# Kernel tuning notes

Hardware: AMD Instinct MI355X
Metric: run time of the kernel (lower is better)

Reference implementation:

```python
import jax, jax.numpy as jnp
import numpy as np
import math

NUM_HEADS = 3
WINDOW = 7


def _shift_masks(ws):
    # row_mask: block mask for windows wrapping across the bottom edge
    half = ws * (ws // 2)  # 21 for ws=7
    row = np.zeros((ws * ws, ws * ws), np.float32)
    row[-half:, :-half] = -np.inf
    row[:-half, -half:] = -np.inf
    # column_mask = rearrange(row, '(r w1) (c w2) -> (w1 r) (w2 c)')
    col = row.reshape(ws, ws, ws, ws).transpose(1, 0, 3, 2).reshape(ws * ws, ws * ws)
    return jnp.asarray(row), jnp.asarray(col)


def setup_inputs() -> dict:
    key = jax.random.key(0)
    ks = jax.random.split(key, 5)
    B, S, E = 64, 3136, 96
    return {
        'x': jax.random.normal(ks[0], (B, S, E), jnp.float32),
        'w1': jax.random.normal(ks[1], (3 * E, E), jnp.float32) * 0.05,
        'b1': jax.random.normal(ks[2], (3 * E,), jnp.float32) * 0.05,
        'w2': jax.random.normal(ks[3], (E, E), jnp.float32) * 0.05,
        'b2': jax.random.normal(ks[4], (E,), jnp.float32) * 0.05,
    }


def reference(x, w1, b1, w2, b2):
    b, S, E = x.shape
    h = w = int(math.sqrt(S))          # 56
    ws = WINDOW
    H = NUM_HEADS
    Eh = E // H                        # head dim = 32
    nh, nw = h // ws, w // ws          # windows per axis = 8
    scale = 1.0 / math.sqrt(E / H)
    # faithful to original: forward shift = -ws//2 = -4, inverse shift = ws//2 = 3
    shift_fwd = -ws // 2
    shift_bwd = ws // 2

    qkv = x @ w1.T + b1                              # [b, S, 3E]
    qkv = qkv.reshape(b, h, w, E, 3)                 # (c K) split, K fastest
    qkv = jnp.roll(qkv, (shift_fwd, shift_fwd), axis=(1, 2))
    # b (nh m1) (nw m2) (H Eh) K -> b H nh nw (m1 m2) Eh K
    qkv = qkv.reshape(b, nh, ws, nw, ws, H, Eh, 3)
    qkv = qkv.transpose(0, 5, 1, 3, 2, 4, 6, 7).reshape(b, H, nh, nw, ws * ws, Eh, 3)
    Q, K, V = qkv[..., 0], qkv[..., 1], qkv[..., 2]

    s = jnp.einsum('bHhwme,bHhwne->bHhwmn', Q, K) * scale  # [b,H,nh,nw,49,49]
    row_mask, col_mask = _shift_masks(ws)
    s = s.at[:, :, -1, :].add(row_mask)   # last row of windows
    s = s.at[:, :, :, -1].add(col_mask)   # last column of windows

    att = jax.nn.softmax(s, axis=-1)
    o = jnp.einsum('bHhwmn,bHhwne->bHhwme', att, V)        # [b,H,nh,nw,49,Eh]
    # b H nh nw (m1 m2) Eh -> b (nh m1) (nw m2) (H Eh)
    o = o.reshape(b, H, nh, nw, ws, ws, Eh)
    o = o.transpose(0, 2, 4, 3, 5, 1, 6).reshape(b, h, w, E)
    o = jnp.roll(o, (shift_bwd, shift_bwd), axis=(1, 2))
    o = o.reshape(b, S, E)
    return o @ w2.T + b2
```

## Files before the change

### kernel.cpp

```cpp
#include <hip/hip_runtime.h>


typedef _Float16 f16;
typedef _Float16 f16x2 __attribute__((ext_vector_type(2)));
typedef _Float16 f16x4 __attribute__((ext_vector_type(4)));
typedef _Float16 f16x8 __attribute__((ext_vector_type(8)));
typedef float f32x4 __attribute__((ext_vector_type(4)));

static __device__ __forceinline__ f32x4 mfma16(f16x8 a, f16x8 b, f32x4 c) {
    return __builtin_amdgcn_mfma_f32_16x16x32_f16(a, b, c, 0, 0, 0);
}
static __device__ __forceinline__ f16x8 cvt8(const float* __restrict__ p) {
    float4 f0 = *(const float4*)(p);
    float4 f1 = *(const float4*)(p + 4);
    f16x8 h;
    h[0]=(f16)f0.x; h[1]=(f16)f0.y; h[2]=(f16)f0.z; h[3]=(f16)f0.w;
    h[4]=(f16)f1.x; h[5]=(f16)f1.y; h[6]=(f16)f1.z; h[7]=(f16)f1.w;
    return h;
}
static __device__ __forceinline__ f16x8 cvt8p(const float4& f0, const float4& f1) {
    f16x8 h;
    h[0]=(f16)f0.x; h[1]=(f16)f0.y; h[2]=(f16)f0.z; h[3]=(f16)f0.w;
    h[4]=(f16)f1.x; h[5]=(f16)f1.y; h[6]=(f16)f1.z; h[7]=(f16)f1.w;
    return h;
}

#define SMEM_BYTES 31152
#define OFF_K  10192
#define OFF_VT 20384

union U2 { int i; f16x2 h; };
union U8 { int i[4]; f16x8 h; };

template<bool WS>
__global__ __launch_bounds__(256, 4) void swin_fused(
    const float* __restrict__ x, const float* __restrict__ w1,
    const float* __restrict__ b1, const float* __restrict__ w2,
    const float* __restrict__ b2, float* __restrict__ out,
    const f16* __restrict__ w1p, const f16* __restrict__ w2p,
    const float* __restrict__ b1p)
{
    __shared__ __align__(16) char smem[SMEM_BYTES];
    f16* q_s  = (f16*)(smem);
    f16* k_s  = (f16*)(smem + OFF_K);
    f16* vt_s = (f16*)(smem + OFF_VT);
    f16* o_s  = q_s;

    const int tid  = threadIdx.x;
    const int wv   = tid >> 6;
    const int lane = tid & 63;
    const int lrow = lane & 15;
    const int lq   = lane >> 4;

    const int bx = blockIdx.x;
    const int b  = bx >> 6;
    const int wz = bx & 63;
    const int wh = wz >> 3;
    const int ww = wz & 7;

    const float* xb = x + b * (3136 * 96);

    if (tid < 96) {
        #pragma unroll
        for (int p7 = 49; p7 < 56; ++p7) vt_s[tid * 56 + p7] = (f16)0.f;
    }
    if (tid < 8) vt_s[96 * 56 + tid] = (f16)0.f;

    {
        f16x8 bf[5][3];
        int   kq[5], cb[5];
        #pragma unroll
        for (int t = 0; t < 5; ++t) {
            int ot = wv + 4 * t;
            if (ot < 18) {
                int kqv = ot / 6;
                kq[t] = kqv;
                cb[t] = (ot - kqv * 6) * 16;
                if constexpr (WS) {
                    #pragma unroll
                    for (int ks = 0; ks < 3; ++ks)
                        bf[t][ks] = *(const f16x8*)(w1p + (ot*16 + lrow)*96 + ks*32 + lq*8);
                } else {
                    int srowA = (ot*16 + lrow - kqv*96) * 3 + kqv;
                    #pragma unroll
                    for (int ks = 0; ks < 3; ++ks)
                        bf[t][ks] = cvt8(w1 + srowA*96 + ks*32 + lq*8);
                }
            } else kq[t] = -1;
        }
        const float* xrow[4];
        #pragma unroll
        for (int pt = 0; pt < 4; ++pt) {
            int p  = pt * 16 + lrow;
            int pc = (p < 49) ? p : 48;
            int i  = pc / 7, j = pc - i * 7;
            int r  = wh * 7 + i + 4; if (r >= 56) r -= 56;
            int c  = ww * 7 + j + 4; if (c >= 56) c -= 56;
            xrow[pt] = xb + (r * 56 + c) * 96;
        }
        float4 xbuf0[3][2], xbuf1[3][2];
        #pragma unroll
        for (int ks = 0; ks < 3; ++ks) {
            xbuf0[ks][0] = *(const float4*)(xrow[0] + ks * 32 + lq * 8);
            xbuf0[ks][1] = *(const float4*)(xrow[0] + ks * 32 + lq * 8 + 4);
        }
        #pragma unroll
        for (int pt = 0; pt < 4; ++pt) {
            float4 (*cur)[2] = (pt & 1) ? xbuf1 : xbuf0;
            float4 (*nxt)[2] = (pt & 1) ? xbuf0 : xbuf1;
            if (pt < 3) {
                #pragma unroll
                for (int ks = 0; ks < 3; ++ks) {
                    nxt[ks][0] = *(const float4*)(xrow[pt+1] + ks * 32 + lq * 8);
                    nxt[ks][1] = *(const float4*)(xrow[pt+1] + ks * 32 + lq * 8 + 4);
                }
            }
            f16x8 xf[3];
            #pragma unroll
            for (int ks = 0; ks < 3; ++ks) xf[ks] = cvt8p(cur[ks][0], cur[ks][1]);
            const int  p   = pt * 16 + lrow;
            const bool pok = (p < 49);
            #pragma unroll
            for (int t = 0; t < 5; ++t) {
                if (kq[t] < 0) continue;
                int ot = wv + 4 * t;
                f32x4 acc = {0.f, 0.f, 0.f, 0.f};
                if (kq[t] == 2) {
                    #pragma unroll
                    for (int ks = 0; ks < 3; ++ks) acc = mfma16(xf[ks], bf[t][ks], acc);
                    float bc;
                    if constexpr (WS) bc = b1p[ot*16 + lrow];
                    else              bc = b1[(ot*16 + lrow - 192)*3 + 2];
                    int cc = cb[t] + lrow;
                    f16x4 pk;
                    #pragma unroll
                    for (int i2 = 0; i2 < 4; ++i2) pk[i2] = (f16)(acc[i2] + bc);
                    int p4 = pt * 16 + lq * 4;
                    if (p4 < 45)       *(f16x4*)(vt_s + cc * 56 + p4) = pk;
                    else if (p4 == 48) vt_s[cc * 56 + 48] = pk[0];
                } else {
                    #pragma unroll
                    for (int ks = 0; ks < 3; ++ks) acc = mfma16(bf[t][ks], xf[ks], acc);
                    if (pok) {
                        f32x4 br;
                        if constexpr (WS) {
                            br = *(const f32x4*)(b1p + ot*16 + lq*4);
                        } else {
                            #pragma unroll
                            for (int i2 = 0; i2 < 4; ++i2)
                                br[i2] = b1[(ot*16 + lq*4 + i2 - kq[t]*96)*3 + kq[t]];
                        }
                        f16x4 pk;
                        #pragma unroll
                        for (int i2 = 0; i2 < 4; ++i2) pk[i2] = (f16)(acc[i2] + br[i2]);
                        f16* dst = (kq[t] == 0 ? q_s : k_s) + p * 104 + cb[t] + lq * 4;
                        *(f16x4*)dst = pk;
                    }
                }
            }
        }
    }
    __syncthreads();

    const bool mrow = (wh == 7), mcol = (ww == 7);
    const float scale = 0.17677669529663687f;
    const int m = wv * 16 + lrow;

    float mv[16];
    {
        const bool am = (m >= 28);
        const bool a4 = (m % 7) >= 4;
        #pragma unroll
        for (int nt = 0; nt < 4; ++nt)
            #pragma unroll
            for (int i2 = 0; i2 < 4; ++i2) {
                int nn = nt * 16 + lq * 4 + i2;
                bool ok = (nn < 49)
                       && (!mrow || (am == (nn >= 28)))
                       && (!mcol || (a4 == ((nn % 7) >= 4)));
                mv[nt*4 + i2] = ok ? 0.f : -3e38f;
            }
    }
    const int idxA = lrow + 32 * (lq & 1);
    const int idxB = idxA + 16;

    f16x8 bq[3];
    #pragma unroll
    for (int hh = 0; hh < 3; ++hh)
        bq[hh] = *(const f16x8*)(q_s + m * 104 + hh * 32 + lq * 8);

    f32x4 sc[4];
    #pragma unroll
    for (int nt = 0; nt < 4; ++nt) {
        f16x8 ak = *(const f16x8*)(k_s + (nt*16 + lrow)*104 + lq*8);
        f32x4 z = {0.f, 0.f, 0.f, 0.f};
        sc[nt] = mfma16(ak, bq[0], z);
    }

    #pragma unroll
    for (int hh = 0; hh < 3; ++hh) {
        f16x8 akn[4];
        if (hh < 2) {
            #pragma unroll
            for (int nt = 0; nt < 4; ++nt)
                akn[nt] = *(const f16x8*)(k_s + (nt*16 + lrow)*104 + (hh+1)*32 + lq*8);
        }
        f16x8 va[2][2];
        #pragma unroll
        for (int et = 0; et < 2; ++et) {
            int vrow = hh * 32 + et * 16 + lrow;
            va[et][0] = *(const f16x8*)(vt_s + vrow * 56 + lq * 8);
            va[et][1] = *(const f16x8*)(vt_s + vrow * 56 + 32 + lq * 8);
        }
        float ev[16];
        #pragma unroll
        for (int nt = 0; nt < 4; ++nt)
            #pragma unroll
            for (int i2 = 0; i2 < 4; ++i2)
                ev[nt*4 + i2] = fmaf(sc[nt][i2], scale, mv[nt*4 + i2]);
        float tm[8];
        #pragma unroll
        for (int k2 = 0; k2 < 8; ++k2) tm[k2] = fmaxf(ev[2*k2], ev[2*k2+1]);
        #pragma unroll
        for (int k2 = 0; k2 < 4; ++k2) tm[k2] = fmaxf(tm[k2], tm[k2+4]);
        float vm = fmaxf(fmaxf(tm[0], tm[1]), fmaxf(tm[2], tm[3]));
        vm = fmaxf(vm, __shfl_xor(vm, 16));
        vm = fmaxf(vm, __shfl_xor(vm, 32));
        #pragma unroll
        for (int k2 = 0; k2 < 16; ++k2) ev[k2] = __expf(ev[k2] - vm);
        float ts[8];
        #pragma unroll
        for (int k2 = 0; k2 < 8; ++k2) ts[k2] = ev[2*k2] + ev[2*k2+1];
        #pragma unroll
        for (int k2 = 0; k2 < 4; ++k2) ts[k2] += ts[k2+4];
        float s = (ts[0] + ts[1]) + (ts[2] + ts[3]);
        s += __shfl_xor(s, 16);
        s += __shfl_xor(s, 32);
        float inv = 1.0f / s;

        int pd[4][2];
        #pragma unroll
        for (int nt = 0; nt < 4; ++nt) {
            U2 u0, u1;
            u0.h[0] = (f16)ev[nt*4+0]; u0.h[1] = (f16)ev[nt*4+1];
            u1.h[0] = (f16)ev[nt*4+2]; u1.h[1] = (f16)ev[nt*4+3];
            pd[nt][0] = u0.i; pd[nt][1] = u1.i;
        }
        U8 ub0, ub1;
        #pragma unroll
        for (int w = 0; w < 4; ++w) {
            int idx = (w < 2) ? idxA : idxB;
            int rr  = w & 1;
            int a0v = __shfl(pd[0][rr], idx);
            int a1v = __shfl(pd[1][rr], idx);
            ub0.i[w] = (lq & 2) ? a1v : a0v;
            int c0v = __shfl(pd[2][rr], idx);
            int c1v = __shfl(pd[3][rr], idx);
            ub1.i[w] = (lq & 2) ? c1v : c0v;
        }
        #pragma unroll
        for (int et = 0; et < 2; ++et) {
            f32x4 z = {0.f, 0.f, 0.f, 0.f};
            f32x4 oc = mfma16(va[et][0], ub0.h, z);
            oc = mfma16(va[et][1], ub1.h, oc);
            if (m < 49) {
                f16x4 pk;
                #pragma unroll
                for (int i2 = 0; i2 < 4; ++i2) pk[i2] = (f16)(oc[i2] * inv);
                *(f16x4*)(o_s + m * 104 + hh * 32 + et * 16 + lq * 4) = pk;
            }
        }
        if (hh < 2) {
            #pragma unroll
            for (int nt = 0; nt < 4; ++nt) {
                f32x4 z = {0.f, 0.f, 0.f, 0.f};
                sc[nt] = mfma16(akn[nt], bq[hh+1], z);
            }
        }
    }

    {
        f16x8 bo[3];
        #pragma unroll
        for (int ks = 0; ks < 3; ++ks)
            bo[ks] = *(const f16x8*)(o_s + m * 104 + ks * 32 + lq * 8);
        int mm2 = (m < 49) ? m : 48;
        int i = mm2 / 7, j = mm2 - i * 7;
        int orow = wh * 7 + i + 3; if (orow >= 56) orow -= 56;
        int ocol = ww * 7 + j + 3; if (ocol >= 56) ocol -= 56;
        float* op = out + (size_t)(b * 3136 + orow * 56 + ocol) * 96;

        f16x8 aw0[3], aw1[3];
        #pragma unroll
        for (int ks = 0; ks < 3; ++ks) {
            if constexpr (WS)
                aw0[ks] = *(const f16x8*)(w2p + lrow*96 + ks*32 + lq*8);
            else
                aw0[ks] = cvt8(w2 + lrow*96 + ks*32 + lq*8);
        }
        #pragma unroll
        for (int ot2 = 0; ot2 < 6; ++ot2) {
            f16x8* cw = (ot2 & 1) ? aw1 : aw0;
            f16x8* nw = (ot2 & 1) ? aw0 : aw1;
            if (ot2 < 5) {
                #pragma unroll
                for (int ks = 0; ks < 3; ++ks) {
                    if constexpr (WS)
                        nw[ks] = *(const f16x8*)(w2p + ((ot2+1)*16 + lrow)*96 + ks*32 + lq*8);
                    else
                        nw[ks] = cvt8(w2 + ((ot2+1)*16 + lrow)*96 + ks*32 + lq*8);
                }
            }
            f32x4 acc = {0.f, 0.f, 0.f, 0.f};
            #pragma unroll
            for (int ks = 0; ks < 3; ++ks) acc = mfma16(cw[ks], bo[ks], acc);
            f32x4 bias = *(const f32x4*)(b2 + ot2 * 16 + lq * 4);
            if (m < 49) {
                f32x4 o4 = acc + bias;
                *(f32x4*)(op + ot2 * 16 + lq * 4) = o4;
            }
        }
    }
}

__global__ void prep_weights(const float* __restrict__ w1, const float* __restrict__ b1,
                             const float* __restrict__ w2,
                             f16* __restrict__ w1p, f16* __restrict__ w2p,
                             float* __restrict__ b1p)
{
    int idx = blockIdx.x * 256 + threadIdx.x;
    if (idx < 27648) {
        int np = idx / 96, k = idx - np * 96;
        int kq = np / 96, c96 = np - kq * 96;
        w1p[idx] = (f16)w1[(c96 * 3 + kq) * 96 + k];
    } else if (idx < 36864) {
        int i2 = idx - 27648;
        w2p[i2] = (f16)w2[i2];
    } else if (idx < 37152) {
        int np = idx - 36864;
        int kq = np / 96, c96 = np - kq * 96;
        b1p[np] = b1[c96 * 3 + kq];
    }
}

extern "C" void kernel_launch(void* const* d_in, const int* in_sizes, int n_in,
                              void* d_out, int out_size, void* d_ws, size_t ws_size,
                              hipStream_t stream) {
    const float* x  = (const float*)d_in[0];
    const float* w1 = (const float*)d_in[1];
    const float* b1 = (const float*)d_in[2];
    const float* w2 = (const float*)d_in[3];
    const float* b2 = (const float*)d_in[4];
    float* out = (float*)d_out;

    const size_t need = 27648u * 2 + 9216u * 2 + 288u * 4;
    if (ws_size >= need) {
        f16*   w1p = (f16*)d_ws;
        f16*   w2p = w1p + 27648;
        float* b1p = (float*)(w2p + 9216);
        prep_weights<<<dim3(146), dim3(256), 0, stream>>>(w1, b1, w2, w1p, w2p, b1p);
        swin_fused<true><<<dim3(4096), dim3(256), 0, stream>>>(
            x, w1, b1, w2, b2, out, w1p, w2p, b1p);
    } else {
        swin_fused<false><<<dim3(4096), dim3(256), 0, stream>>>(
            x, w1, b1, w2, b2, out, nullptr, nullptr, nullptr);
    }
}
```

Measured before the change: 238.4 us.

## Fuse per-head output projection into attention loop and change LDS row strides

The output projection is now accumulated head by head inside the attention loop. As soon as a head's 32 output channels are written to shared memory, they are multiplied against the matching 32-column slice of w2 into six persistent accumulators, replacing the separate projection phase at the end. Separately, the Q/K row stride is changed from 104 to 100 halves and the V-transpose stride from 56 to 60, to cut LDS bank conflicts and shave shared memory. The risks are the six extra live accumulator registers under a 4-waves-per-SIMD launch bound, and 16-byte LDS vector accesses that are no longer 16-byte aligned with the new strides.

```diff
diff --git a/kernel.cpp b/kernel.cpp
--- a/kernel.cpp
+++ b/kernel.cpp
@@ -25,9 +25,11 @@
     return h;
 }
 
-#define SMEM_BYTES 31152
-#define OFF_K  10192
-#define OFF_VT 20384
+#define QK_STR 100
+#define VT_STR 60
+#define SMEM_BYTES 31136
+#define OFF_K  9800
+#define OFF_VT 19600
 
 union U2 { int i; f16x2 h; };
 union U8 { int i[4]; f16x8 h; };
@@ -62,9 +64,9 @@
 
     if (tid < 96) {
         #pragma unroll
-        for (int p7 = 49; p7 < 56; ++p7) vt_s[tid * 56 + p7] = (f16)0.f;
-    }
-    if (tid < 8) vt_s[96 * 56 + tid] = (f16)0.f;
+        for (int p7 = 49; p7 < 60; ++p7) vt_s[tid * VT_STR + p7] = (f16)0.f;
+    }
+    if (tid < 8) vt_s[96 * VT_STR + tid] = (f16)0.f;
 
     {
         f16x8 bf[5][3];
@@ -136,8 +138,8 @@
                     #pragma unroll
                     for (int i2 = 0; i2 < 4; ++i2) pk[i2] = (f16)(acc[i2] + bc);
                     int p4 = pt * 16 + lq * 4;
-                    if (p4 < 45)       *(f16x4*)(vt_s + cc * 56 + p4) = pk;
-                    else if (p4 == 48) vt_s[cc * 56 + 48] = pk[0];
+                    if (p4 < 45)       *(f16x4*)(vt_s + cc * VT_STR + p4) = pk;
+                    else if (p4 == 48) vt_s[cc * VT_STR + 48] = pk[0];
                 } else {
                     #pragma unroll
                     for (int ks = 0; ks < 3; ++ks) acc = mfma16(bf[t][ks], xf[ks], acc);
@@ -153,7 +155,7 @@
                         f16x4 pk;
                         #pragma unroll
                         for (int i2 = 0; i2 < 4; ++i2) pk[i2] = (f16)(acc[i2] + br[i2]);
-                        f16* dst = (kq[t] == 0 ? q_s : k_s) + p * 104 + cb[t] + lq * 4;
+                        f16* dst = (kq[t] == 0 ? q_s : k_s) + p * QK_STR + cb[t] + lq * 4;
                         *(f16x4*)dst = pk;
                     }
                 }
@@ -187,12 +189,16 @@
     f16x8 bq[3];
     #pragma unroll
     for (int hh = 0; hh < 3; ++hh)
-        bq[hh] = *(const f16x8*)(q_s + m * 104 + hh * 32 + lq * 8);
+        bq[hh] = *(const f16x8*)(q_s + m * QK_STR + hh * 32 + lq * 8);
+
+    f32x4 acc2[6];
+    #pragma unroll
+    for (int ot2 = 0; ot2 < 6; ++ot2) acc2[ot2] = f32x4{0.f, 0.f, 0.f, 0.f};
 
     f32x4 sc[4];
     #pragma unroll
     for (int nt = 0; nt < 4; ++nt) {
-        f16x8 ak = *(const f16x8*)(k_s + (nt*16 + lrow)*104 + lq*8);
+        f16x8 ak = *(const f16x8*)(k_s + (nt*16 + lrow)*QK_STR + lq*8);
         f32x4 z = {0.f, 0.f, 0.f, 0.f};
         sc[nt] = mfma16(ak, bq[0], z);
     }
@@ -203,14 +209,14 @@
         if (hh < 2) {
             #pragma unroll
             for (int nt = 0; nt < 4; ++nt)
-                akn[nt] = *(const f16x8*)(k_s + (nt*16 + lrow)*104 + (hh+1)*32 + lq*8);
+                akn[nt] = *(const f16x8*)(k_s + (nt*16 + lrow)*QK_STR + (hh+1)*32 + lq*8);
         }
         f16x8 va[2][2];
         #pragma unroll
         for (int et = 0; et < 2; ++et) {
             int vrow = hh * 32 + et * 16 + lrow;
-            va[et][0] = *(const f16x8*)(vt_s + vrow * 56 + lq * 8);
-            va[et][1] = *(const f16x8*)(vt_s + vrow * 56 + 32 + lq * 8);
+            va[et][0] = *(const f16x8*)(vt_s + vrow * VT_STR + lq * 8);
+            va[et][1] = *(const f16x8*)(vt_s + vrow * VT_STR + 32 + lq * 8);
         }
         float ev[16];
         #pragma unroll
@@ -267,8 +273,22 @@
                 f16x4 pk;
                 #pragma unroll
                 for (int i2 = 0; i2 < 4; ++i2) pk[i2] = (f16)(oc[i2] * inv);
-                *(f16x4*)(o_s + m * 104 + hh * 32 + et * 16 + lq * 4) = pk;
-            }
+                *(f16x4*)(o_s + m * QK_STR + hh * 32 + et * 16 + lq * 4) = pk;
+            }
+        }
+        {
+            f16x8 aw_h[6];
+            #pragma unroll
+            for (int ot2 = 0; ot2 < 6; ++ot2) {
+                if constexpr (WS)
+                    aw_h[ot2] = *(const f16x8*)(w2p + (ot2*16 + lrow)*96 + hh*32 + lq*8);
+                else
+                    aw_h[ot2] = cvt8(w2 + (ot2*16 + lrow)*96 + hh*32 + lq*8);
+            }
+            f16x8 bo_h = *(const f16x8*)(o_s + m * QK_STR + hh * 32 + lq * 8);
+            #pragma unroll
+            for (int ot2 = 0; ot2 < 6; ++ot2)
+                acc2[ot2] = mfma16(aw_h[ot2], bo_h, acc2[ot2]);
         }
         if (hh < 2) {
             #pragma unroll
@@ -280,43 +300,16 @@
     }
 
     {
-        f16x8 bo[3];
-        #pragma unroll
-        for (int ks = 0; ks < 3; ++ks)
-            bo[ks] = *(const f16x8*)(o_s + m * 104 + ks * 32 + lq * 8);
         int mm2 = (m < 49) ? m : 48;
         int i = mm2 / 7, j = mm2 - i * 7;
         int orow = wh * 7 + i + 3; if (orow >= 56) orow -= 56;
         int ocol = ww * 7 + j + 3; if (ocol >= 56) ocol -= 56;
         float* op = out + (size_t)(b * 3136 + orow * 56 + ocol) * 96;
-
-        f16x8 aw0[3], aw1[3];
-        #pragma unroll
-        for (int ks = 0; ks < 3; ++ks) {
-            if constexpr (WS)
-                aw0[ks] = *(const f16x8*)(w2p + lrow*96 + ks*32 + lq*8);
-            else
-                aw0[ks] = cvt8(w2 + lrow*96 + ks*32 + lq*8);
-        }
         #pragma unroll
         for (int ot2 = 0; ot2 < 6; ++ot2) {
-            f16x8* cw = (ot2 & 1) ? aw1 : aw0;
-            f16x8* nw = (ot2 & 1) ? aw0 : aw1;
-            if (ot2 < 5) {
-                #pragma unroll
-                for (int ks = 0; ks < 3; ++ks) {
-                    if constexpr (WS)
-                        nw[ks] = *(const f16x8*)(w2p + ((ot2+1)*16 + lrow)*96 + ks*32 + lq*8);
-                    else
-                        nw[ks] = cvt8(w2 + ((ot2+1)*16 + lrow)*96 + ks*32 + lq*8);
-                }
-            }
-            f32x4 acc = {0.f, 0.f, 0.f, 0.f};
-            #pragma unroll
-            for (int ks = 0; ks < 3; ++ks) acc = mfma16(cw[ks], bo[ks], acc);
             f32x4 bias = *(const f32x4*)(b2 + ot2 * 16 + lq * 4);
             if (m < 49) {
-                f32x4 o4 = acc + bias;
+                f32x4 o4 = acc2[ot2] + bias;
                 *(f32x4*)(op + ot2 * 16 + lq * 4) = o4;
             }
         }
```

After: 254.9 us. +6.9%, slower.
